# Performance work log

Measured on AMD Instinct MI355X. Metric: run time of the kernel, lower is better.

## Reference

```python
import jax, jax.numpy as jnp
import numpy as np

B, T, X, E, H, L = 4096, 32, 256, 32, 512, 2  # batch, theta_size, x_size, n_masks, hidden, num_hidden_layers


def _prelu(v, a):
    # PReLU with per-channel slope a (broadcast [E,H] or [B,E,H] vs [B,E,H])
    return jnp.where(v >= 0, v, a * v)


def setup_inputs() -> dict:
    key = jax.random.key(0)
    ks = jax.random.split(key, 12)
    theta = jax.random.normal(ks[0], (B, T), dtype=jnp.float32)
    x = jax.random.normal(ks[1], (B, X), dtype=jnp.float32)
    masks = jax.random.randint(ks[2], (E, T), 0, 2, dtype=jnp.int32)
    masks = masks.at[:, 0].set(1)  # guarantee non-empty subsets
    D = T + X
    s_in = 1.0 / np.sqrt(D)
    s_h = 1.0 / np.sqrt(H)
    # first Linear, split into theta-part and x-part of the weight matrix
    W1t = jax.random.normal(ks[3], (E, T, H), dtype=jnp.float32) * s_in
    W1x = jax.random.normal(ks[4], (E, X, H), dtype=jnp.float32) * s_in
    b1 = jax.random.normal(ks[5], (E, H), dtype=jnp.float32) * s_in
    a1 = jnp.full((E, H), 0.25, dtype=jnp.float32)  # PReLU init
    # num_layers hidden Linear(H,H) + PReLU
    Wh = jax.random.normal(ks[6], (L, E, H, H), dtype=jnp.float32) * s_h
    bh = jax.random.normal(ks[7], (L, E, H), dtype=jnp.float32) * s_h
    ah = jnp.full((L, E, H), 0.25, dtype=jnp.float32)
    # output Linear(H, 1) -> squeeze(-1)
    Wo = jax.random.normal(ks[8], (E, H), dtype=jnp.float32) * s_h
    bo = jax.random.normal(ks[9], (E,), dtype=jnp.float32) * s_h
    return {"theta": theta, "x": x, "masks": masks, "W1t": W1t, "W1x": W1x,
            "b1": b1, "a1": a1, "Wh": Wh, "bh": bh, "ah": ah, "Wo": Wo, "bo": bo}


def reference(theta, x, masks, W1t, W1x, b1, a1, Wh, bh, ah, Wo, bo):
    # theta[..., mask] followed by Linear is equivalent to masking theta per
    # expert and contracting with the full per-expert theta weight block.
    m = masks.astype(theta.dtype)                      # [E, T]
    tm = theta[:, None, :] * m[None, :, :]             # [B, E, T]
    h = (jnp.einsum('bet,eth->beh', tm, W1t)
         + jnp.einsum('bx,exh->beh', x, W1x) + b1)     # [B, E, H]
    h = _prelu(h, a1)
    for i in range(Wh.shape[0]):                       # small fixed layer loop
        h = jnp.einsum('beh,ehk->bek', h, Wh[i]) + bh[i]
        h = _prelu(h, ah[i])
    # Linear(H,1).squeeze(-1), stacked over masks on the last dim -> [B, E]
    return jnp.einsum('beh,eh->be', h, Wo) + bo
```

## Files before the change

### kernel.cpp

```cpp
#include <hip/hip_runtime.h>
#include <stdint.h>

#define B_SZ 4096
#define T_SZ 32
#define X_SZ 256
#define E_SZ 32
#define H_SZ 512
#define BM   64
#define AROW 1040
#define D_SZ 288

typedef __attribute__((ext_vector_type(8))) short  short8;
typedef __attribute__((ext_vector_type(4))) float  floatx4;

__device__ __forceinline__ unsigned short f2bf(float f) {
  unsigned u = __float_as_uint(f);
  u += 0x7fffu + ((u >> 16) & 1u);
  return (unsigned short)(u >> 16);
}
__device__ __forceinline__ unsigned pk2(float a, float b) {
  return (unsigned)f2bf(a) | ((unsigned)f2bf(b) << 16);
}

#define LPITCH 526

__global__ __launch_bounds__(256) void prep5_kernel(
    const float* __restrict__ W1t, const float* __restrict__ W1x,
    const int* __restrict__ masks, const float* __restrict__ Wh,
    const float* __restrict__ theta, const float* __restrict__ x,
    uint4* __restrict__ wcat, uint4* __restrict__ whf,
    unsigned short* __restrict__ tx) {
  const int bid = blockIdx.x, t = threadIdx.x;
  if (bid >= 1312) {
    int g = bid - 1312;
    int r = g * 64 + (t >> 2), c = t & 3;
    {
      float4 a = *(const float4*)(theta + (size_t)r * T_SZ + c * 8);
      float4 b = *(const float4*)(theta + (size_t)r * T_SZ + c * 8 + 4);
      *(uint4*)(tx + (size_t)r * D_SZ + c * 8) =
          make_uint4(pk2(a.x, a.y), pk2(a.z, a.w), pk2(b.x, b.y), pk2(b.z, b.w));
    }
#pragma unroll
    for (int j = 0; j < 8; ++j) {
      float4 a = *(const float4*)(x + (size_t)r * X_SZ + c * 64 + j * 8);
      float4 b = *(const float4*)(x + (size_t)r * X_SZ + c * 64 + j * 8 + 4);
      *(uint4*)(tx + (size_t)r * D_SZ + T_SZ + c * 64 + j * 8) =
          make_uint4(pk2(a.x, a.y), pk2(a.z, a.w), pk2(b.x, b.y), pk2(b.z, b.w));
    }
    return;
  }
  __shared__ unsigned short lds[32 * LPITCH];
  const int xcd = bid & 7, j = bid >> 3;
  const int q41 = j / 41;
  const int c   = j - q41 * 41;
  const int e   = xcd * 4 + (3 - q41);
  float4 v[16];
  if (c < 9) {
#pragma unroll
    for (int p = 0; p < 16; ++p) {
      int f  = p * 256 + t;
      int kk = f >> 7, n = (f & 127) * 4;
      int k  = c * 32 + kk;
      if (k < T_SZ) {
        v[p] = *(const float4*)(W1t + ((size_t)e * T_SZ + k) * H_SZ + n);
        float m = (float)masks[e * T_SZ + k];
        v[p].x *= m; v[p].y *= m; v[p].z *= m; v[p].w *= m;
      } else {
        v[p] = *(const float4*)(W1x + ((size_t)e * X_SZ + (k - T_SZ)) * H_SZ + n);
      }
    }
  } else {
    int h = c - 9, le = h >> 4, kt = h & 15;
    const float* base = Wh + (size_t)(le * E_SZ + e) * H_SZ * H_SZ +
                        (size_t)kt * 32 * H_SZ;
#pragma unroll
    for (int p = 0; p < 16; ++p) {
      int f  = p * 256 + t;
      int kk = f >> 7, n = (f & 127) * 4;
      v[p] = *(const float4*)(base + (size_t)kk * H_SZ + n);
    }
  }
  unsigned* lds32 = (unsigned*)lds;
#pragma unroll
  for (int p = 0; p < 16; ++p) {
    int f  = p * 256 + t;
    int kk = f >> 7, n = (f & 127) * 4;
    int di = (kk * LPITCH + n) >> 1;
    lds32[di]     = pk2(v[p].x, v[p].y);
    lds32[di + 1] = pk2(v[p].z, v[p].w);
  }
  __syncthreads();
  uint4* dst = (c < 9)
                   ? (wcat + ((size_t)e * 9 + c) * 2048)
                   : (whf + ((size_t)(((c - 9) >> 4) * E_SZ + e) * 16 +
                             ((c - 9) & 15)) * 2048);
#pragma unroll 2
  for (int p = 0; p < 8; ++p) {
    int u  = p * 256 + t;
    int nb = u >> 6, l = u & 63;
    int n  = nb * 16 + (l & 15);
    int k0 = (l >> 4) * 8;
    unsigned d[4];
#pragma unroll
    for (int jj = 0; jj < 4; ++jj) {
      unsigned lo = lds[(k0 + 2 * jj)     * LPITCH + n];
      unsigned hi = lds[(k0 + 2 * jj + 1) * LPITCH + n];
      d[jj] = lo | (hi << 16);
    }
    dst[u] = make_uint4(d[0], d[1], d[2], d[3]);
  }
}

template <int NKT>
__device__ __forceinline__ void gemm_run(const char* smA, const short8* wp,
                                         int l16, int quad,
                                         floatx4 (&acc)[4][4]) {
#pragma unroll
  for (int mb = 0; mb < 4; ++mb)
#pragma unroll
    for (int i = 0; i < 4; ++i) acc[mb][i] = (floatx4)(0.f);
  short8 b[2][4], a[2][4];
#pragma unroll
  for (int i = 0; i < 4; ++i) b[0][i] = wp[i * 64];
#pragma unroll
  for (int mb = 0; mb < 4; ++mb)
    a[0][mb] = *(const short8*)(smA + (mb * 16 + l16) * AROW + quad * 16);
#pragma unroll
  for (int kt = 0; kt < NKT; ++kt) {
    const int cur = kt & 1, nxt = cur ^ 1;
    const int kn  = (kt + 1 < NKT) ? kt + 1 : kt;
#pragma unroll
    for (int i = 0; i < 4; ++i) b[nxt][i] = wp[(size_t)kn * 2048 + i * 64];
#pragma unroll
    for (int mb = 0; mb < 4; ++mb)
      a[nxt][mb] =
          *(const short8*)(smA + (mb * 16 + l16) * AROW + kn * 64 + quad * 16);
#pragma unroll
    for (int mb = 0; mb < 4; ++mb)
#pragma unroll
      for (int i = 0; i < 4; ++i)
        acc[mb][i] = __builtin_amdgcn_mfma_f32_16x16x32_bf16(a[cur][mb],
                                                             b[cur][i],
                                                             acc[mb][i], 0, 0, 0);
  }
}

__global__ __launch_bounds__(512, 4) void mlp_kernel(
    const unsigned short* __restrict__ tx,
    const short8* __restrict__ wcat, const short8* __restrict__ whf,
    const float* __restrict__ b1, const float* __restrict__ a1,
    const float* __restrict__ bh, const float* __restrict__ ah,
    const float* __restrict__ Wo, const float* __restrict__ bo,
    float* __restrict__ out) {
  __shared__ __align__(16) char smA[BM * AROW];
  const int tid = threadIdx.x;
  const int bid = blockIdx.x;
  const int m0  = (bid >> 3) * BM;
  const int w   = tid >> 6, l = tid & 63, l16 = l & 15, quad = l >> 4;

  floatx4 acc[4][4];

  auto epi_store = [&](const float* bias, const float* slope) {
    float bb[4], aa[4];
#pragma unroll
    for (int i = 0; i < 4; ++i) {
      int col = w * 64 + i * 16 + l16;
      bb[i] = bias[col];
      aa[i] = slope[col];
    }
    __syncthreads();
#pragma unroll
    for (int mb = 0; mb < 4; ++mb) {
#pragma unroll
      for (int i = 0; i < 4; ++i) {
        unsigned dw[4];
#pragma unroll
        for (int r = 0; r < 4; ++r) {
          float v = acc[mb][i][r] + bb[i];
          v = v >= 0.f ? v : aa[i] * v;
          float o  = __shfl_xor(v, 1, 64);
          float lo = (l16 & 1) ? o : v;
          float hi = (l16 & 1) ? v : o;
          dw[r] = pk2(lo, hi);
        }
        int col2  = w * 64 + i * 16 + (l16 & ~1);
        int rbase = (l16 & 1) * 2;
#pragma unroll
        for (int rr = 0; rr < 2; ++rr) {
          int row = mb * 16 + quad * 4 + rbase + rr;
          *(unsigned*)(smA + row * AROW + col2 * 2) = dw[rbase + rr];
        }
      }
    }
    __syncthreads();
  };

  const int woff = w * 256 + l;
#pragma unroll 1
  for (int p = 0; p < 4; ++p) {
    const int e = (bid & 7) * 4 + p;
    __syncthreads();
    {
      int r = tid >> 3, c = tid & 7;
      const unsigned short* src = tx + (size_t)(m0 + r) * D_SZ;
#pragma unroll
      for (int q = 0; q < 9; ++q)
        *(uint2*)(smA + r * AROW + 8 * (c + 8 * q)) =
            *(const uint2*)(src + 4 * (c + 8 * q));
    }
    __syncthreads();

    gemm_run<9>(smA, wcat + (size_t)e * 9 * 2048 + woff, l16, quad, acc);
    epi_store(b1 + (size_t)e * H_SZ, a1 + (size_t)e * H_SZ);
    gemm_run<16>(smA, whf + (size_t)e * 16 * 2048 + woff, l16, quad, acc);
    epi_store(bh + (size_t)e * H_SZ, ah + (size_t)e * H_SZ);
    gemm_run<16>(smA, whf + (size_t)(E_SZ + e) * 16 * 2048 + woff, l16, quad,
                 acc);
    {
      float bb[4], aa[4], wo[4];
#pragma unroll
      for (int i = 0; i < 4; ++i) {
        int col = w * 64 + i * 16 + l16;
        bb[i] = bh[(size_t)(E_SZ + e) * H_SZ + col];
        aa[i] = ah[(size_t)(E_SZ + e) * H_SZ + col];
        wo[i] = Wo[(size_t)e * H_SZ + col];
      }
      float ps[4][4];
#pragma unroll
      for (int mb = 0; mb < 4; ++mb)
#pragma unroll
        for (int r = 0; r < 4; ++r) ps[mb][r] = 0.f;
#pragma unroll
      for (int mb = 0; mb < 4; ++mb)
#pragma unroll
        for (int i = 0; i < 4; ++i)
#pragma unroll
          for (int r = 0; r < 4; ++r) {
            float v = acc[mb][i][r] + bb[i];
            v = v >= 0.f ? v : aa[i] * v;
            ps[mb][r] += v * wo[i];
          }
#pragma unroll
      for (int d = 1; d < 16; d <<= 1)
#pragma unroll
        for (int mb = 0; mb < 4; ++mb)
#pragma unroll
          for (int r = 0; r < 4; ++r) ps[mb][r] += __shfl_xor(ps[mb][r], d, 64);
      __syncthreads();
      float* scratch = (float*)smA;
      if (l16 == 0) {
#pragma unroll
        for (int mb = 0; mb < 4; ++mb)
#pragma unroll
          for (int r = 0; r < 4; ++r)
            scratch[(mb * 16 + quad * 4 + r) * 8 + w] = ps[mb][r];
      }
      __syncthreads();
      if (tid < BM) {
        float s = 0.f;
#pragma unroll
        for (int ww = 0; ww < 8; ++ww) s += scratch[tid * 8 + ww];
        out[(size_t)(m0 + tid) * E_SZ + e] = s + bo[e];
      }
    }
  }
}

extern "C" void kernel_launch(void* const* d_in, const int* in_sizes, int n_in,
                              void* d_out, int out_size, void* d_ws, size_t ws_size,
                              hipStream_t stream) {
  const float* theta = (const float*)d_in[0];
  const float* x     = (const float*)d_in[1];
  const int*   masks = (const int*)d_in[2];
  const float* W1t   = (const float*)d_in[3];
  const float* W1x   = (const float*)d_in[4];
  const float* b1    = (const float*)d_in[5];
  const float* a1    = (const float*)d_in[6];
  const float* Wh    = (const float*)d_in[7];
  const float* bh    = (const float*)d_in[8];
  const float* ah    = (const float*)d_in[9];
  const float* Wo    = (const float*)d_in[10];
  const float* bo    = (const float*)d_in[11];
  float* out = (float*)d_out;

  uint4* wcat = (uint4*)d_ws;
  uint4* whf  = (uint4*)((char*)d_ws + (size_t)E_SZ * 9 * 2048 * 16);
  unsigned short* tx =
      (unsigned short*)((char*)d_ws + (size_t)E_SZ * 9 * 2048 * 16 +
                        (size_t)2 * E_SZ * 16 * 2048 * 16);

  prep5_kernel<<<1376, 256, 0, stream>>>(W1t, W1x, masks, Wh, theta, x,
                                         wcat, whf, tx);
  mlp_kernel<<<512, 512, 0, stream>>>(tx, (const short8*)wcat,
                                      (const short8*)whf, b1, a1, bh, ah, Wo,
                                      bo, out);
}
```

Baseline: 364.6 us.

## Switch to 32x32x16 MFMA and one expert per block across 2048 blocks

Replaces the 16x16x32 bf16 MFMA tiles with 32x32x16 MFMA tiles and relays out the prepacked weights to match the new B-fragment layout. Each block now handles a single expert instead of looping over four, so the grid grows to 2048 blocks and the input tile load happens once per block. The final layer goes through the same bf16 epilogue into shared memory, followed by a row-wise dot product with Wo. This aims to cut LDS A-fragment traffic per MFMA and improve scheduling, at the cost of more block launches and rounding the last hidden layer to bf16 before the output projection.

```diff
diff --git a/kernel.cpp b/kernel.cpp
--- a/kernel.cpp
+++ b/kernel.cpp
@@ -10,8 +10,8 @@
 #define AROW 1040
 #define D_SZ 288
 
-typedef __attribute__((ext_vector_type(8))) short  short8;
-typedef __attribute__((ext_vector_type(4))) float  floatx4;
+typedef __attribute__((ext_vector_type(8)))  short short8;
+typedef __attribute__((ext_vector_type(16))) float floatx16;
 
 __device__ __forceinline__ unsigned short f2bf(float f) {
   unsigned u = __float_as_uint(f);
@@ -24,7 +24,7 @@
 
 #define LPITCH 526
 
-__global__ __launch_bounds__(256) void prep5_kernel(
+__global__ __launch_bounds__(256) void prep6_kernel(
     const float* __restrict__ W1t, const float* __restrict__ W1x,
     const int* __restrict__ masks, const float* __restrict__ Wh,
     const float* __restrict__ theta, const float* __restrict__ x,
@@ -97,9 +97,9 @@
 #pragma unroll 2
   for (int p = 0; p < 8; ++p) {
     int u  = p * 256 + t;
-    int nb = u >> 6, l = u & 63;
-    int n  = nb * 16 + (l & 15);
-    int k0 = (l >> 4) * 8;
+    int nt = u >> 7, s = (u >> 6) & 1, l = u & 63;
+    int n  = nt * 32 + (l & 31);
+    int k0 = s * 16 + (l >> 5) * 8;
     unsigned d[4];
 #pragma unroll
     for (int jj = 0; jj < 4; ++jj) {
@@ -112,36 +112,37 @@
 }
 
 template <int NKT>
-__device__ __forceinline__ void gemm_run(const char* smA, const short8* wp,
-                                         int l16, int quad,
-                                         floatx4 (&acc)[4][4]) {
-#pragma unroll
-  for (int mb = 0; mb < 4; ++mb)
-#pragma unroll
-    for (int i = 0; i < 4; ++i) acc[mb][i] = (floatx4)(0.f);
-  short8 b[2][4], a[2][4];
+__device__ __forceinline__ void gemm32(const char* smA, const short8* wp,
+                                       int l, floatx16 (&acc)[2][2]) {
+  const int l31 = l & 31, lh = l >> 5;
+#pragma unroll
+  for (int mt = 0; mt < 2; ++mt)
+#pragma unroll
+    for (int j = 0; j < 2; ++j) acc[mt][j] = (floatx16)(0.f);
+  short8 b[2][4];
 #pragma unroll
   for (int i = 0; i < 4; ++i) b[0][i] = wp[i * 64];
-#pragma unroll
-  for (int mb = 0; mb < 4; ++mb)
-    a[0][mb] = *(const short8*)(smA + (mb * 16 + l16) * AROW + quad * 16);
 #pragma unroll
   for (int kt = 0; kt < NKT; ++kt) {
     const int cur = kt & 1, nxt = cur ^ 1;
     const int kn  = (kt + 1 < NKT) ? kt + 1 : kt;
 #pragma unroll
     for (int i = 0; i < 4; ++i) b[nxt][i] = wp[(size_t)kn * 2048 + i * 64];
-#pragma unroll
-    for (int mb = 0; mb < 4; ++mb)
-      a[nxt][mb] =
-          *(const short8*)(smA + (mb * 16 + l16) * AROW + kn * 64 + quad * 16);
-#pragma unroll
-    for (int mb = 0; mb < 4; ++mb)
-#pragma unroll
-      for (int i = 0; i < 4; ++i)
-        acc[mb][i] = __builtin_amdgcn_mfma_f32_16x16x32_bf16(a[cur][mb],
-                                                             b[cur][i],
-                                                             acc[mb][i], 0, 0, 0);
+    short8 a[2][2];
+#pragma unroll
+    for (int mt = 0; mt < 2; ++mt)
+#pragma unroll
+      for (int s = 0; s < 2; ++s)
+        a[mt][s] = *(const short8*)(smA + (mt * 32 + l31) * AROW + kt * 64 +
+                                    s * 32 + lh * 16);
+#pragma unroll
+    for (int mt = 0; mt < 2; ++mt)
+#pragma unroll
+      for (int j = 0; j < 2; ++j)
+#pragma unroll
+        for (int s = 0; s < 2; ++s)
+          acc[mt][j] = __builtin_amdgcn_mfma_f32_32x32x16_bf16(
+              a[mt][s], b[cur][j * 2 + s], acc[mt][j], 0, 0, 0);
   }
 }
 
@@ -155,40 +156,52 @@
   __shared__ __align__(16) char smA[BM * AROW];
   const int tid = threadIdx.x;
   const int bid = blockIdx.x;
-  const int m0  = (bid >> 3) * BM;
-  const int w   = tid >> 6, l = tid & 63, l16 = l & 15, quad = l >> 4;
-
-  floatx4 acc[4][4];
+  const int e   = (bid & 7) * 4 + (bid >> 9);
+  const int m0  = ((bid >> 3) & 63) * BM;
+  const int w   = tid >> 6, l = tid & 63, l31 = l & 31, lh = l >> 5;
+
+  {
+    int r = tid >> 3, c = tid & 7;
+    const unsigned short* src = tx + (size_t)(m0 + r) * D_SZ;
+#pragma unroll
+    for (int q = 0; q < 9; ++q)
+      *(uint2*)(smA + r * AROW + 8 * (c + 8 * q)) =
+          *(const uint2*)(src + 4 * (c + 8 * q));
+  }
+  __syncthreads();
+
+  floatx16 acc[2][2];
 
   auto epi_store = [&](const float* bias, const float* slope) {
-    float bb[4], aa[4];
-#pragma unroll
-    for (int i = 0; i < 4; ++i) {
-      int col = w * 64 + i * 16 + l16;
-      bb[i] = bias[col];
-      aa[i] = slope[col];
+    float bb[2], aa[2];
+#pragma unroll
+    for (int j = 0; j < 2; ++j) {
+      int col = w * 64 + j * 32 + l31;
+      bb[j] = bias[col];
+      aa[j] = slope[col];
     }
     __syncthreads();
 #pragma unroll
-    for (int mb = 0; mb < 4; ++mb) {
-#pragma unroll
-      for (int i = 0; i < 4; ++i) {
-        unsigned dw[4];
-#pragma unroll
-        for (int r = 0; r < 4; ++r) {
-          float v = acc[mb][i][r] + bb[i];
-          v = v >= 0.f ? v : aa[i] * v;
+    for (int mt = 0; mt < 2; ++mt) {
+#pragma unroll
+      for (int j = 0; j < 2; ++j) {
+        unsigned dw[16];
+#pragma unroll
+        for (int r = 0; r < 16; ++r) {
+          float v = acc[mt][j][r] + bb[j];
+          v = v >= 0.f ? v : aa[j] * v;
           float o  = __shfl_xor(v, 1, 64);
-          float lo = (l16 & 1) ? o : v;
-          float hi = (l16 & 1) ? v : o;
+          float lo = (l & 1) ? o : v;
+          float hi = (l & 1) ? v : o;
           dw[r] = pk2(lo, hi);
         }
-        int col2  = w * 64 + i * 16 + (l16 & ~1);
-        int rbase = (l16 & 1) * 2;
-#pragma unroll
-        for (int rr = 0; rr < 2; ++rr) {
-          int row = mb * 16 + quad * 4 + rbase + rr;
-          *(unsigned*)(smA + row * AROW + col2 * 2) = dw[rbase + rr];
+        int col2  = w * 64 + j * 32 + (l31 & ~1);
+        int rbase = (l & 1) * 8;
+#pragma unroll
+        for (int rr = 0; rr < 8; ++rr) {
+          int r   = rbase + rr;
+          int row = mt * 32 + (r & 3) + 8 * (r >> 2) + 4 * lh;
+          *(unsigned*)(smA + row * AROW + col2 * 2) = dw[r];
         }
       }
     }
@@ -196,73 +209,33 @@
   };
 
   const int woff = w * 256 + l;
-#pragma unroll 1
-  for (int p = 0; p < 4; ++p) {
-    const int e = (bid & 7) * 4 + p;
-    __syncthreads();
-    {
-      int r = tid >> 3, c = tid & 7;
-      const unsigned short* src = tx + (size_t)(m0 + r) * D_SZ;
-#pragma unroll
-      for (int q = 0; q < 9; ++q)
-        *(uint2*)(smA + r * AROW + 8 * (c + 8 * q)) =
-            *(const uint2*)(src + 4 * (c + 8 * q));
-    }
-    __syncthreads();
-
-    gemm_run<9>(smA, wcat + (size_t)e * 9 * 2048 + woff, l16, quad, acc);
-    epi_store(b1 + (size_t)e * H_SZ, a1 + (size_t)e * H_SZ);
-    gemm_run<16>(smA, whf + (size_t)e * 16 * 2048 + woff, l16, quad, acc);
-    epi_store(bh + (size_t)e * H_SZ, ah + (size_t)e * H_SZ);
-    gemm_run<16>(smA, whf + (size_t)(E_SZ + e) * 16 * 2048 + woff, l16, quad,
-                 acc);
-    {
-      float bb[4], aa[4], wo[4];
-#pragma unroll
-      for (int i = 0; i < 4; ++i) {
-        int col = w * 64 + i * 16 + l16;
-        bb[i] = bh[(size_t)(E_SZ + e) * H_SZ + col];
-        aa[i] = ah[(size_t)(E_SZ + e) * H_SZ + col];
-        wo[i] = Wo[(size_t)e * H_SZ + col];
+  gemm32<9>(smA, wcat + (size_t)e * 9 * 2048 + woff, l, acc);
+  epi_store(b1 + (size_t)e * H_SZ, a1 + (size_t)e * H_SZ);
+  gemm32<16>(smA, whf + (size_t)e * 16 * 2048 + woff, l, acc);
+  epi_store(bh + (size_t)e * H_SZ, ah + (size_t)e * H_SZ);
+  gemm32<16>(smA, whf + (size_t)(E_SZ + e) * 16 * 2048 + woff, l, acc);
+  epi_store(bh + (size_t)(E_SZ + e) * H_SZ, ah + (size_t)(E_SZ + e) * H_SZ);
+  {
+    int row = tid >> 3, c8 = tid & 7;
+    float s = 0.f;
+    const float* wo = Wo + (size_t)e * H_SZ;
+#pragma unroll
+    for (int j = 0; j < 8; ++j) {
+      int colb = c8 * 16 + j * 128;
+      short8 av = *(const short8*)(smA + row * AROW + colb);
+      int col   = c8 * 8 + j * 64;
+      float4 w0 = *(const float4*)(wo + col);
+      float4 w1 = *(const float4*)(wo + col + 4);
+      float wv[8] = {w0.x, w0.y, w0.z, w0.w, w1.x, w1.y, w1.z, w1.w};
+#pragma unroll
+      for (int k = 0; k < 8; ++k) {
+        float av_f = __uint_as_float(((unsigned)(unsigned short)av[k]) << 16);
+        s += av_f * wv[k];
       }
-      float ps[4][4];
-#pragma unroll
-      for (int mb = 0; mb < 4; ++mb)
-#pragma unroll
-        for (int r = 0; r < 4; ++r) ps[mb][r] = 0.f;
-#pragma unroll
-      for (int mb = 0; mb < 4; ++mb)
-#pragma unroll
-        for (int i = 0; i < 4; ++i)
-#pragma unroll
-          for (int r = 0; r < 4; ++r) {
-            float v = acc[mb][i][r] + bb[i];
-            v = v >= 0.f ? v : aa[i] * v;
-            ps[mb][r] += v * wo[i];
-          }
-#pragma unroll
-      for (int d = 1; d < 16; d <<= 1)
-#pragma unroll
-        for (int mb = 0; mb < 4; ++mb)
-#pragma unroll
-          for (int r = 0; r < 4; ++r) ps[mb][r] += __shfl_xor(ps[mb][r], d, 64);
-      __syncthreads();
-      float* scratch = (float*)smA;
-      if (l16 == 0) {
-#pragma unroll
-        for (int mb = 0; mb < 4; ++mb)
-#pragma unroll
-          for (int r = 0; r < 4; ++r)
-            scratch[(mb * 16 + quad * 4 + r) * 8 + w] = ps[mb][r];
-      }
-      __syncthreads();
-      if (tid < BM) {
-        float s = 0.f;
-#pragma unroll
-        for (int ww = 0; ww < 8; ++ww) s += scratch[tid * 8 + ww];
-        out[(size_t)(m0 + tid) * E_SZ + e] = s + bo[e];
-      }
-    }
+    }
+#pragma unroll
+    for (int d = 1; d < 8; d <<= 1) s += __shfl_xor(s, d, 64);
+    if (c8 == 0) out[(size_t)(m0 + row) * E_SZ + e] = s + bo[e];
   }
 }
 
@@ -289,9 +262,9 @@
       (unsigned short*)((char*)d_ws + (size_t)E_SZ * 9 * 2048 * 16 +
                         (size_t)2 * E_SZ * 16 * 2048 * 16);
 
-  prep5_kernel<<<1376, 256, 0, stream>>>(W1t, W1x, masks, Wh, theta, x,
+  prep6_kernel<<<1376, 256, 0, stream>>>(W1t, W1x, masks, Wh, theta, x,
                                          wcat, whf, tx);
-  mlp_kernel<<<512, 512, 0, stream>>>(tx, (const short8*)wcat,
-                                      (const short8*)whf, b1, a1, bh, ah, Wo,
-                                      bo, out);
-}
+  mlp_kernel<<<2048, 512, 0, stream>>>(tx, (const short8*)wcat,
+                                       (const short8*)whf, b1, a1, bh, ah, Wo,
+                                       bo, out);
+}
```

New measurement: 474.9 us. 30.3% more time.
